# Kernel tuning notes

Hardware: AMD Instinct MI355X
Metric: run time of the kernel (lower is better)

Reference implementation:

```python
import jax, jax.numpy as jnp
import numpy as np

H = 128
B, N, K = 2, 16384, 16


def _gather_neighbors(a, idx):
    # a: (B,N,D), idx: (B,N,K) -> (B,N,K,D), per-batch gather along N
    return jax.vmap(lambda ab, ib: ab[ib])(a, idx)


def setup_inputs() -> dict:
    key = jax.random.key(0)
    ks = jax.random.split(key, 16)
    def lin(k, fan_in, shape):
        lim = 1.0 / np.sqrt(fan_in)
        return jax.random.uniform(k, shape, jnp.float32, -lim, lim)
    inp = {
        'h': jax.random.normal(ks[0], (B, N, H), jnp.float32),
        'x': jax.random.normal(ks[1], (B, N, 3), jnp.float32),
        'edge_idx': jax.random.randint(ks[2], (B, N, K), 0, N),
        # edge_mlp: Linear(2H+1->H), SiLU, Linear(H->H), SiLU
        'We1': lin(ks[3], 2 * H + 1, (2 * H + 1, H)), 'be1': lin(ks[4], 2 * H + 1, (H,)),
        'We2': lin(ks[5], H, (H, H)), 'be2': lin(ks[6], H, (H,)),
        # coord_mlp: Linear(H->H), SiLU, Linear(H->1, no bias)
        'Wc1': lin(ks[7], H, (H, H)), 'bc1': lin(ks[8], H, (H,)),
        'Wc2': lin(ks[9], H, (H, 1)),
        # node_mlp: Linear(2H->H), SiLU, Linear(H->H)
        'Wn1': lin(ks[10], 2 * H, (2 * H, H)), 'bn1': lin(ks[11], 2 * H, (H,)),
        'Wn2': lin(ks[12], H, (H, H)), 'bn2': lin(ks[13], H, (H,)),
    }
    return inp


def reference(h, x, edge_idx, We1, be1, We2, be2, Wc1, bc1, Wc2, Wn1, bn1, Wn2, bn2):
    k = edge_idx.shape[2]
    h_neigh = _gather_neighbors(h, edge_idx)          # (B,N,K,H)
    x_neigh = _gather_neighbors(x, edge_idx)          # (B,N,K,3)
    x_diff = x[:, :, None, :] - x_neigh               # (B,N,K,3)
    sq_dist = jnp.sum(x_diff * x_diff, axis=-1, keepdims=True)  # (B,N,K,1)
    h_i = jnp.broadcast_to(h[:, :, None, :], h_neigh.shape)
    edge_feat = jnp.concatenate([h_i, h_neigh, sq_dist], axis=-1)  # (B,N,K,2H+1)
    m_ij = jax.nn.silu(jax.nn.silu(edge_feat @ We1 + be1) @ We2 + be2)  # (B,N,K,H)
    coord_w = jax.nn.silu(m_ij @ Wc1 + bc1) @ Wc2     # (B,N,K,1)
    x_new = x + jnp.mean(x_diff * coord_w, axis=2)    # (B,N,3)
    m_i = jnp.sum(m_ij, axis=2)                       # (B,N,H)
    node_in = jnp.concatenate([h, m_i], axis=-1)      # (B,N,2H)
    h_new = jax.nn.silu(node_in @ Wn1 + bn1) @ Wn2 + bn2 + h
    return (h_new, x_new)
```

## Files before the change

kernel.cpp:

```cpp
#include <hip/hip_runtime.h>
#include <math.h>

#define H 128
#define KN 16
#define NN 16384
#define NB 8
#define EB 128

typedef short s16x8 __attribute__((ext_vector_type(8)));
typedef float f32x4 __attribute__((ext_vector_type(4)));

__device__ __forceinline__ float b2f(ushort u){
    union { uint i; float f; } v; v.i = ((uint)u) << 16; return v.f;
}
__device__ __forceinline__ ushort f2b(float f){
    union { float f; uint i; } v; v.f = f;
    uint r = v.i + 0x7fffu + ((v.i >> 16) & 1u);
    return (ushort)(r >> 16);
}
__device__ __forceinline__ float silu_f(float v){
    float e = __expf(-v);
    return v * __builtin_amdgcn_rcpf(1.0f + e);
}

__global__ __launch_bounds__(256) void pack_all(
    const float* __restrict__ We2, const float* __restrict__ Wc1,
    const float* __restrict__ Wn1, const float* __restrict__ Wn2,
    const float* __restrict__ We1,
    ushort* __restrict__ dWe2, ushort* __restrict__ dWc1,
    ushort* __restrict__ dWn1, ushort* __restrict__ dWn2,
    ushort* __restrict__ dW1p)
{
    int idx = blockIdx.x * 256 + threadIdx.x;
    int fid = idx >> 6, l = idx & 63;
    const float* src; ushort* dst; int Kt; int mode = 0; int lfid;
    if (fid < 32)       { src = We2; dst = dWe2; Kt = 4; lfid = fid; }
    else if (fid < 64)  { src = Wc1; dst = dWc1; Kt = 4; lfid = fid - 64 + 32 - 32; lfid = fid - 32; }
    else if (fid < 128) { src = Wn1; dst = dWn1; Kt = 8; lfid = fid - 64; }
    else if (fid < 160) { src = Wn2; dst = dWn2; Kt = 4; lfid = fid - 128; }
    else                { src = We1; dst = dW1p; Kt = 4; mode = 1; lfid = fid - 160; }
    int mt = lfid / Kt, kt = lfid % Kt;
    int m = mt * 16 + (l & 15);
    s16x8 ov;
#pragma unroll
    for (int e = 0; e < 8; e++){
        int k = kt * 32 + ((l >> 4) << 3) + e;
        float v;
        if (mode == 0) v = src[k * 128 + m];
        else           v = src[(k + ((m >= 128) ? 128 : 0)) * 128 + (m & 127)];
        ov[e] = (short)f2b(v);
    }
    *(s16x8*)(dst + (size_t)lfid * 512 + l * 8) = ov;
}

__global__ __launch_bounds__(256) void precompute_mfma(
    const float* __restrict__ h, const float* __restrict__ be1,
    const ushort* __restrict__ W1p,
    ushort* __restrict__ A, ushort* __restrict__ Bm)
{
    const int tid = threadIdx.x;
    const int w = tid >> 6, l = tid & 63, lg = l >> 4, li = l & 15;
    const int i0 = blockIdx.x * 64;

    f32x4 acc[4][4];
#pragma unroll
    for (int a = 0; a < 4; a++)
#pragma unroll
        for (int b = 0; b < 4; b++){ acc[a][b][0]=0.f; acc[a][b][1]=0.f; acc[a][b][2]=0.f; acc[a][b][3]=0.f; }

    for (int nt = 0; nt < 4; nt++){
        int node = i0 + nt * 16 + li;
        const float* hp = h + (size_t)node * 128 + lg * 8;
        s16x8 bfr[4];
#pragma unroll
        for (int kt = 0; kt < 4; kt++){
            float4 v0 = *(const float4*)(hp + kt * 32);
            float4 v1 = *(const float4*)(hp + kt * 32 + 4);
            s16x8 bf;
            bf[0]=(short)f2b(v0.x); bf[1]=(short)f2b(v0.y); bf[2]=(short)f2b(v0.z); bf[3]=(short)f2b(v0.w);
            bf[4]=(short)f2b(v1.x); bf[5]=(short)f2b(v1.y); bf[6]=(short)f2b(v1.z); bf[7]=(short)f2b(v1.w);
            bfr[kt] = bf;
        }
#pragma unroll
        for (int mtl = 0; mtl < 4; mtl++){
            int mt = w * 4 + mtl;
#pragma unroll
            for (int kt = 0; kt < 4; kt++){
                s16x8 af = *(const s16x8*)(W1p + (size_t)(mt * 4 + kt) * 512 + l * 8);
                acc[mtl][nt] = __builtin_amdgcn_mfma_f32_16x16x32_bf16(af, bfr[kt], acc[mtl][nt], 0, 0, 0);
            }
        }
    }
#pragma unroll
    for (int mtl = 0; mtl < 4; mtl++){
        int mt = w * 4 + mtl;
        int ccb = mt * 16 + lg * 4;
#pragma unroll
        for (int nt = 0; nt < 4; nt++){
            int node = i0 + nt * 16 + li;
            float b0=0.f,b1=0.f,b2=0.f,b3=0.f;
            if (ccb < 128){ float4 bb = *(const float4*)(be1 + ccb); b0=bb.x; b1=bb.y; b2=bb.z; b3=bb.w; }
            ushort o0 = f2b(acc[mtl][nt][0] + b0);
            ushort o1 = f2b(acc[mtl][nt][1] + b1);
            ushort o2 = f2b(acc[mtl][nt][2] + b2);
            ushort o3 = f2b(acc[mtl][nt][3] + b3);
            uint2 val = make_uint2((uint)o0 | ((uint)o1 << 16), (uint)o2 | ((uint)o3 << 16));
            ushort* dst = (ccb < 128) ? (A + (size_t)node * 128 + ccb)
                                      : (Bm + (size_t)node * 128 + (ccb - 128));
            *(uint2*)dst = val;
        }
    }
}

__global__ __launch_bounds__(256, 3) void egnn_fused(
    const float* __restrict__ h, const float* __restrict__ x,
    const int* __restrict__ edge_idx,
    const ushort* __restrict__ A, const ushort* __restrict__ Bm,
    const float* __restrict__ We1,
    const ushort* __restrict__ We2T, const float* __restrict__ be2,
    const ushort* __restrict__ Wc1T, const float* __restrict__ bc1,
    const float* __restrict__ Wc2,
    const ushort* __restrict__ Wn1T, const float* __restrict__ bn1,
    const ushort* __restrict__ Wn2T, const float* __restrict__ bn2,
    float* __restrict__ out, int BN)
{
    __shared__ ushort m_lds[EB * 128];
    __shared__ float  hsh[NB * 132];
    __shared__ ushort Ash[NB * 128];
    __shared__ float  msum[NB * 132];
    __shared__ ushort u_lds[16 * 128];
    __shared__ ushort w256sh[128];
    __shared__ float  sqd[EB];
    __shared__ float  xd[EB * 3];
    __shared__ float  cwvp[4][EB];
    __shared__ int    jgs[EB];

    const int tid = threadIdx.x;
    const int w = tid >> 6, l = tid & 63, lg = l >> 4, li = l & 15;
    const int i0 = blockIdx.x * NB;

    {
        int r = tid >> 5, c = (tid & 31) * 4;
        *(float4*)&hsh[r * 132 + c] = *(const float4*)&h[(size_t)(i0 + r) * 128 + c];
        if (tid < 128){
            int rr = tid >> 4, cc = (tid & 15) * 8;
            *(s16x8*)&Ash[rr * 128 + cc] = *(const s16x8*)&A[(size_t)(i0 + rr) * 128 + cc];
        } else {
            int t2 = tid - 128;
            w256sh[t2] = f2b(We1[256 * 128 + t2]);
            s16x8 z; for (int e = 0; e < 8; e++) z[e] = 0;
            *(s16x8*)&u_lds[(8 + (t2 >> 4)) * 128 + (t2 & 15) * 8] = z;
        }
        if (tid < EB){
            int e = tid;
            int i = i0 + (e >> 4);
            int b = i / NN;
            int jl = edge_idx[(size_t)i * KN + (e & 15)];
            int j = b * NN + jl;
            jgs[e] = j;
            float d0 = x[i*3+0] - x[j*3+0];
            float d1 = x[i*3+1] - x[j*3+1];
            float d2 = x[i*3+2] - x[j*3+2];
            xd[e*3+0] = d0; xd[e*3+1] = d1; xd[e*3+2] = d2;
            sqd[e] = d0*d0 + d1*d1 + d2*d2;
        }
    }
    __syncthreads();

    {
        const int e0 = w * 32;
#pragma unroll
        for (int nt = 0; nt < 2; nt++){
            int edge = e0 + nt * 16 + li;
            int nodel = edge >> 4;
            int j = jgs[edge];
            float sq = sqd[edge];
#pragma unroll
            for (int kt = 0; kt < 4; kt++){
                int c8 = kt * 32 + lg * 8;
                s16x8 bm = *(const s16x8*)&Bm[(size_t)j * 128 + c8];
                s16x8 av = *(const s16x8*)&Ash[nodel * 128 + c8];
                s16x8 wv = *(const s16x8*)&w256sh[c8];
                s16x8 ov;
#pragma unroll
                for (int e = 0; e < 8; e++){
                    float t = b2f((ushort)av[e]) + b2f((ushort)bm[e]) + sq * b2f((ushort)wv[e]);
                    ov[e] = (short)f2b(silu_f(t));
                }
                int blk = (kt * 4 + lg) ^ (edge & 7);
                *(s16x8*)&m_lds[edge * 128 + blk * 8] = ov;
            }
        }
    }
    __syncthreads();

    f32x4 acc[16];
#pragma unroll
    for (int q = 0; q < 16; q++){ acc[q][0]=0.f; acc[q][1]=0.f; acc[q][2]=0.f; acc[q][3]=0.f; }

#pragma unroll
    for (int kt = 0; kt < 4; kt++){
        s16x8 bfr[8];
#pragma unroll
        for (int nt = 0; nt < 8; nt++){
            int edge = nt * 16 + li;
            int blk = (kt * 4 + lg) ^ (edge & 7);
            bfr[nt] = *(const s16x8*)&m_lds[edge * 128 + blk * 8];
        }
#pragma unroll
        for (int mtl = 0; mtl < 2; mtl++){
            int mt = w * 2 + mtl;
            s16x8 af = *(const s16x8*)&We2T[(size_t)(mt * 4 + kt) * 512 + l * 8];
#pragma unroll
            for (int nt = 0; nt < 8; nt++)
                acc[mtl * 8 + nt] = __builtin_amdgcn_mfma_f32_16x16x32_bf16(af, bfr[nt], acc[mtl * 8 + nt], 0, 0, 0);
        }
    }
    __syncthreads();

#pragma unroll
    for (int mtl = 0; mtl < 2; mtl++){
        int mt = w * 2 + mtl;
        int cb = mt * 16 + lg * 4;
        float4 bb = *(const float4*)&be2[cb];
#pragma unroll
        for (int nt = 0; nt < 8; nt++){
            int edge = nt * 16 + li;
            f32x4 a = acc[mtl * 8 + nt];
            ushort o0 = f2b(silu_f(a[0] + bb.x));
            ushort o1 = f2b(silu_f(a[1] + bb.y));
            ushort o2 = f2b(silu_f(a[2] + bb.z));
            ushort o3 = f2b(silu_f(a[3] + bb.w));
            int blk = (mt * 2 + (lg >> 1)) ^ (edge & 7);
            uint2 val = make_uint2((uint)o0 | ((uint)o1 << 16), (uint)o2 | ((uint)o3 << 16));
            *(uint2*)&m_lds[edge * 128 + blk * 8 + (lg & 1) * 4] = val;
        }
    }
    {
        int nodel = l >> 3;
        int c0 = w * 32 + (l & 7) * 4;
        float s0=0.f, s1=0.f, s2=0.f, s3=0.f;
#pragma unroll
        for (int k = 0; k < 16; k++){
            int edge = nodel * 16 + k;
            int blk = (c0 >> 3) ^ (edge & 7);
            uint2 v = *(uint2*)&m_lds[edge * 128 + blk * 8 + (c0 & 4)];
            s0 += b2f((ushort)(v.x & 0xffff)); s1 += b2f((ushort)(v.x >> 16));
            s2 += b2f((ushort)(v.y & 0xffff)); s3 += b2f((ushort)(v.y >> 16));
        }
        float4 sv = make_float4(s0, s1, s2, s3);
        *(float4*)&msum[nodel * 132 + c0] = sv;
    }
    __syncthreads();

#pragma unroll
    for (int q = 0; q < 16; q++){ acc[q][0]=0.f; acc[q][1]=0.f; acc[q][2]=0.f; acc[q][3]=0.f; }
#pragma unroll
    for (int kt = 0; kt < 4; kt++){
        s16x8 bfr[8];
#pragma unroll
        for (int nt = 0; nt < 8; nt++){
            int edge = nt * 16 + li;
            int blk = (kt * 4 + lg) ^ (edge & 7);
            bfr[nt] = *(const s16x8*)&m_lds[edge * 128 + blk * 8];
        }
#pragma unroll
        for (int mtl = 0; mtl < 2; mtl++){
            int mt = w * 2 + mtl;
            s16x8 af = *(const s16x8*)&Wc1T[(size_t)(mt * 4 + kt) * 512 + l * 8];
#pragma unroll
            for (int nt = 0; nt < 8; nt++)
                acc[mtl * 8 + nt] = __builtin_amdgcn_mfma_f32_16x16x32_bf16(af, bfr[nt], acc[mtl * 8 + nt], 0, 0, 0);
        }
    }
    {
        float cwp[8];
#pragma unroll
        for (int nt = 0; nt < 8; nt++) cwp[nt] = 0.f;
#pragma unroll
        for (int mtl = 0; mtl < 2; mtl++){
            int mt = w * 2 + mtl;
            int cb = mt * 16 + lg * 4;
            float4 bc = *(const float4*)&bc1[cb];
            float4 wc = *(const float4*)&Wc2[cb];
#pragma unroll
            for (int nt = 0; nt < 8; nt++){
                f32x4 a = acc[mtl * 8 + nt];
                cwp[nt] += silu_f(a[0] + bc.x) * wc.x + silu_f(a[1] + bc.y) * wc.y
                         + silu_f(a[2] + bc.z) * wc.z + silu_f(a[3] + bc.w) * wc.w;
            }
        }
#pragma unroll
        for (int nt = 0; nt < 8; nt++){
            float v = cwp[nt];
            v += __shfl_xor(v, 16);
            v += __shfl_xor(v, 32);
            if (lg == 0) cwvp[w][nt * 16 + li] = v;
        }
    }

    {
        f32x4 acc3[2];
        acc3[0][0]=0.f; acc3[0][1]=0.f; acc3[0][2]=0.f; acc3[0][3]=0.f;
        acc3[1][0]=0.f; acc3[1][1]=0.f; acc3[1][2]=0.f; acc3[1][3]=0.f;
#pragma unroll
        for (int kt = 0; kt < 8; kt++){
            int node = li & 7;
            const float* bp = (kt < 4) ? (hsh + node * 132 + kt * 32 + lg * 8)
                                       : (msum + node * 132 + (kt - 4) * 32 + lg * 8);
            float4 v0 = *(const float4*)bp;
            float4 v1 = *(const float4*)(bp + 4);
            s16x8 bf;
            bf[0]=(short)f2b(v0.x); bf[1]=(short)f2b(v0.y); bf[2]=(short)f2b(v0.z); bf[3]=(short)f2b(v0.w);
            bf[4]=(short)f2b(v1.x); bf[5]=(short)f2b(v1.y); bf[6]=(short)f2b(v1.z); bf[7]=(short)f2b(v1.w);
#pragma unroll
            for (int mtl = 0; mtl < 2; mtl++){
                int mt = w * 2 + mtl;
                s16x8 af = *(const s16x8*)&Wn1T[(size_t)(mt * 8 + kt) * 512 + l * 8];
                acc3[mtl] = __builtin_amdgcn_mfma_f32_16x16x32_bf16(af, bf, acc3[mtl], 0, 0, 0);
            }
        }
#pragma unroll
        for (int mtl = 0; mtl < 2; mtl++){
            int mt = w * 2 + mtl;
            int cb = mt * 16 + lg * 4;
            float4 bb = *(const float4*)&bn1[cb];
            if (li < 8){
                f32x4 a = acc3[mtl];
                ushort o0 = f2b(silu_f(a[0] + bb.x));
                ushort o1 = f2b(silu_f(a[1] + bb.y));
                ushort o2 = f2b(silu_f(a[2] + bb.z));
                ushort o3 = f2b(silu_f(a[3] + bb.w));
                int blk = (mt * 2 + (lg >> 1)) ^ (li & 7);
                uint2 val = make_uint2((uint)o0 | ((uint)o1 << 16), (uint)o2 | ((uint)o3 << 16));
                *(uint2*)&u_lds[li * 128 + blk * 8 + (lg & 1) * 4] = val;
            }
        }
    }
    __syncthreads();

    if (tid < 24){
        int nd = tid / 3, d = tid % 3;
        float s = 0.f;
#pragma unroll
        for (int k = 0; k < 16; k++){
            int e = nd * 16 + k;
            s += xd[e * 3 + d] * (cwvp[0][e] + cwvp[1][e] + cwvp[2][e] + cwvp[3][e]);
        }
        int i = i0 + nd;
        out[(size_t)BN * H + (size_t)i * 3 + d] = x[(size_t)i * 3 + d] + s * (1.0f / 16.0f);
    }

    {
        f32x4 acc4[2];
        acc4[0][0]=0.f; acc4[0][1]=0.f; acc4[0][2]=0.f; acc4[0][3]=0.f;
        acc4[1][0]=0.f; acc4[1][1]=0.f; acc4[1][2]=0.f; acc4[1][3]=0.f;
#pragma unroll
        for (int kt = 0; kt < 4; kt++){
            int blk = (kt * 4 + lg) ^ (li & 7);
            s16x8 bf = *(const s16x8*)&u_lds[li * 128 + blk * 8];
#pragma unroll
            for (int mtl = 0; mtl < 2; mtl++){
                int mt = w * 2 + mtl;
                s16x8 af = *(const s16x8*)&Wn2T[(size_t)(mt * 4 + kt) * 512 + l * 8];
                acc4[mtl] = __builtin_amdgcn_mfma_f32_16x16x32_bf16(af, bf, acc4[mtl], 0, 0, 0);
            }
        }
#pragma unroll
        for (int mtl = 0; mtl < 2; mtl++){
            int mt = w * 2 + mtl;
            int cb = mt * 16 + lg * 4;
            if (li < 8){
                float4 bb = *(const float4*)&bn2[cb];
                float4 hv = *(const float4*)&hsh[li * 132 + cb];
                f32x4 a = acc4[mtl];
                float4 o;
                o.x = a[0] + bb.x + hv.x;
                o.y = a[1] + bb.y + hv.y;
                o.z = a[2] + bb.z + hv.z;
                o.w = a[3] + bb.w + hv.w;
                *(float4*)&out[(size_t)(i0 + li) * 128 + cb] = o;
            }
        }
    }
}

extern "C" void kernel_launch(void* const* d_in, const int* in_sizes, int n_in,
                              void* d_out, int out_size, void* d_ws, size_t ws_size,
                              hipStream_t stream) {
    const float* h        = (const float*)d_in[0];
    const float* x        = (const float*)d_in[1];
    const int*   edge_idx = (const int*)d_in[2];
    const float* We1      = (const float*)d_in[3];
    const float* be1      = (const float*)d_in[4];
    const float* We2      = (const float*)d_in[5];
    const float* be2      = (const float*)d_in[6];
    const float* Wc1      = (const float*)d_in[7];
    const float* bc1      = (const float*)d_in[8];
    const float* Wc2      = (const float*)d_in[9];
    const float* Wn1      = (const float*)d_in[10];
    const float* bn1      = (const float*)d_in[11];
    const float* Wn2      = (const float*)d_in[12];
    const float* bn2      = (const float*)d_in[13];
    float* out = (float*)d_out;

    const int BN = in_sizes[0] / H;

    ushort* A    = (ushort*)d_ws;
    ushort* Bm   = A + (size_t)BN * H;
    ushort* We2T = Bm + (size_t)BN * H;
    ushort* Wc1T = We2T + 32 * 512;
    ushort* Wn1T = Wc1T + 32 * 512;
    ushort* Wn2T = Wn1T + 64 * 512;
    ushort* W1pT = Wn2T + 32 * 512;

    pack_all<<<56, 256, 0, stream>>>(We2, Wc1, Wn1, Wn2, We1,
                                     We2T, Wc1T, Wn1T, Wn2T, W1pT);
    precompute_mfma<<<BN / 64, 256, 0, stream>>>(h, be1, W1pT, A, Bm);
    egnn_fused<<<BN / NB, 256, 0, stream>>>(h, x, edge_idx, A, Bm, We1,
                                            We2T, be2, Wc1T, bc1, Wc2,
                                            Wn1T, bn1, Wn2T, bn2, out, BN);
}
```

Before: 127.5 us.

## Shrink and alias LDS buffers, store bf16 staging, raise occupancy to 4 waves

```diff
diff --git a/kernel.cpp b/kernel.cpp
--- a/kernel.cpp
+++ b/kernel.cpp
@@ -1,4 +1,5 @@
 #include <hip/hip_runtime.h>
+#include <hip/hip_bf16.h>
 #include <math.h>
 
 #define H 128
@@ -6,17 +7,24 @@
 #define NN 16384
 #define NB 8
 #define EB 128
+#define HS 136
 
 typedef short s16x8 __attribute__((ext_vector_type(8)));
 typedef float f32x4 __attribute__((ext_vector_type(4)));
 
-__device__ __forceinline__ float b2f(ushort u){
-    union { uint i; float f; } v; v.i = ((uint)u) << 16; return v.f;
-}
-__device__ __forceinline__ ushort f2b(float f){
-    union { float f; uint i; } v; v.f = f;
-    uint r = v.i + 0x7fffu + ((v.i >> 16) & 1u);
-    return (ushort)(r >> 16);
+__device__ __forceinline__ float u2f_lo(uint u){
+    union { uint i; float f; } v; v.i = u << 16; return v.f;
+}
+__device__ __forceinline__ float u2f_hi(uint u){
+    union { uint i; float f; } v; v.i = u & 0xffff0000u; return v.f;
+}
+__device__ __forceinline__ uint pk2(float lo, float hi){
+    __hip_bfloat162 b = __float22bfloat162_rn(float2{lo, hi});
+    uint u; __builtin_memcpy(&u, &b, 4); return u;
+}
+__device__ __forceinline__ ushort f2b1(float f){
+    __hip_bfloat16 b = __float2bfloat16(f);
+    ushort u; __builtin_memcpy(&u, &b, 2); return u;
 }
 __device__ __forceinline__ float silu_f(float v){
     float e = __expf(-v);
@@ -35,7 +43,7 @@
     int fid = idx >> 6, l = idx & 63;
     const float* src; ushort* dst; int Kt; int mode = 0; int lfid;
     if (fid < 32)       { src = We2; dst = dWe2; Kt = 4; lfid = fid; }
-    else if (fid < 64)  { src = Wc1; dst = dWc1; Kt = 4; lfid = fid - 64 + 32 - 32; lfid = fid - 32; }
+    else if (fid < 64)  { src = Wc1; dst = dWc1; Kt = 4; lfid = fid - 32; }
     else if (fid < 128) { src = Wn1; dst = dWn1; Kt = 8; lfid = fid - 64; }
     else if (fid < 160) { src = Wn2; dst = dWn2; Kt = 4; lfid = fid - 128; }
     else                { src = We1; dst = dW1p; Kt = 4; mode = 1; lfid = fid - 160; }
@@ -48,7 +56,7 @@
         float v;
         if (mode == 0) v = src[k * 128 + m];
         else           v = src[(k + ((m >= 128) ? 128 : 0)) * 128 + (m & 127)];
-        ov[e] = (short)f2b(v);
+        ov[e] = (short)f2b1(v);
     }
     *(s16x8*)(dst + (size_t)lfid * 512 + l * 8) = ov;
 }
@@ -76,9 +84,9 @@
         for (int kt = 0; kt < 4; kt++){
             float4 v0 = *(const float4*)(hp + kt * 32);
             float4 v1 = *(const float4*)(hp + kt * 32 + 4);
-            s16x8 bf;
-            bf[0]=(short)f2b(v0.x); bf[1]=(short)f2b(v0.y); bf[2]=(short)f2b(v0.z); bf[3]=(short)f2b(v0.w);
-            bf[4]=(short)f2b(v1.x); bf[5]=(short)f2b(v1.y); bf[6]=(short)f2b(v1.z); bf[7]=(short)f2b(v1.w);
+            uint4 uu = make_uint4(pk2(v0.x, v0.y), pk2(v0.z, v0.w),
+                                  pk2(v1.x, v1.y), pk2(v1.z, v1.w));
+            s16x8 bf; __builtin_memcpy(&bf, &uu, 16);
             bfr[kt] = bf;
         }
 #pragma unroll
@@ -100,11 +108,8 @@
             int node = i0 + nt * 16 + li;
             float b0=0.f,b1=0.f,b2=0.f,b3=0.f;
             if (ccb < 128){ float4 bb = *(const float4*)(be1 + ccb); b0=bb.x; b1=bb.y; b2=bb.z; b3=bb.w; }
-            ushort o0 = f2b(acc[mtl][nt][0] + b0);
-            ushort o1 = f2b(acc[mtl][nt][1] + b1);
-            ushort o2 = f2b(acc[mtl][nt][2] + b2);
-            ushort o3 = f2b(acc[mtl][nt][3] + b3);
-            uint2 val = make_uint2((uint)o0 | ((uint)o1 << 16), (uint)o2 | ((uint)o3 << 16));
+            uint2 val = make_uint2(pk2(acc[mtl][nt][0] + b0, acc[mtl][nt][1] + b1),
+                                   pk2(acc[mtl][nt][2] + b2, acc[mtl][nt][3] + b3));
             ushort* dst = (ccb < 128) ? (A + (size_t)node * 128 + ccb)
                                       : (Bm + (size_t)node * 128 + (ccb - 128));
             *(uint2*)dst = val;
@@ -112,7 +117,7 @@
     }
 }
 
-__global__ __launch_bounds__(256, 3) void egnn_fused(
+__global__ __launch_bounds__(256, 4) void egnn_fused(
     const float* __restrict__ h, const float* __restrict__ x,
     const int* __restrict__ edge_idx,
     const ushort* __restrict__ A, const ushort* __restrict__ Bm,
@@ -124,16 +129,16 @@
     const ushort* __restrict__ Wn2T, const float* __restrict__ bn2,
     float* __restrict__ out, int BN)
 {
-    __shared__ ushort m_lds[EB * 128];
-    __shared__ float  hsh[NB * 132];
-    __shared__ ushort Ash[NB * 128];
-    __shared__ float  msum[NB * 132];
-    __shared__ ushort u_lds[16 * 128];
-    __shared__ ushort w256sh[128];
+    __shared__ __align__(16) ushort m_lds[EB * 128];
+    __shared__ __align__(16) uint   AshCw[512];
+    __shared__ __align__(16) ushort hsh_bf[NB * HS];
+    __shared__ __align__(16) ushort msum_bf[NB * HS];
+    __shared__ __align__(16) ushort w256sh[128];
     __shared__ float  sqd[EB];
-    __shared__ float  xd[EB * 3];
-    __shared__ float  cwvp[4][EB];
     __shared__ int    jgs[EB];
+
+    ushort* Ash = (ushort*)AshCw;
+    float (*cwvp)[EB] = (float(*)[EB])AshCw;
 
     const int tid = threadIdx.x;
     const int w = tid >> 6, l = tid & 63, lg = l >> 4, li = l & 15;
@@ -141,15 +146,14 @@
 
     {
         int r = tid >> 5, c = (tid & 31) * 4;
-        *(float4*)&hsh[r * 132 + c] = *(const float4*)&h[(size_t)(i0 + r) * 128 + c];
+        float4 hv = *(const float4*)&h[(size_t)(i0 + r) * 128 + c];
+        *(uint2*)&hsh_bf[r * HS + c] = make_uint2(pk2(hv.x, hv.y), pk2(hv.z, hv.w));
         if (tid < 128){
             int rr = tid >> 4, cc = (tid & 15) * 8;
-            *(s16x8*)&Ash[rr * 128 + cc] = *(const s16x8*)&A[(size_t)(i0 + rr) * 128 + cc];
+            *(uint4*)&Ash[rr * 128 + cc] = *(const uint4*)&A[(size_t)(i0 + rr) * 128 + cc];
         } else {
             int t2 = tid - 128;
-            w256sh[t2] = f2b(We1[256 * 128 + t2]);
-            s16x8 z; for (int e = 0; e < 8; e++) z[e] = 0;
-            *(s16x8*)&u_lds[(8 + (t2 >> 4)) * 128 + (t2 & 15) * 8] = z;
+            w256sh[t2] = f2b1(We1[256 * 128 + t2]);
         }
         if (tid < EB){
             int e = tid;
@@ -158,10 +162,9 @@
             int jl = edge_idx[(size_t)i * KN + (e & 15)];
             int j = b * NN + jl;
             jgs[e] = j;
-            float d0 = x[i*3+0] - x[j*3+0];
-            float d1 = x[i*3+1] - x[j*3+1];
-            float d2 = x[i*3+2] - x[j*3+2];
-            xd[e*3+0] = d0; xd[e*3+1] = d1; xd[e*3+2] = d2;
+            float d0 = x[(size_t)i*3+0] - x[(size_t)j*3+0];
+            float d1 = x[(size_t)i*3+1] - x[(size_t)j*3+1];
+            float d2 = x[(size_t)i*3+2] - x[(size_t)j*3+2];
             sqd[e] = d0*d0 + d1*d1 + d2*d2;
         }
     }
@@ -178,17 +181,21 @@
 #pragma unroll
             for (int kt = 0; kt < 4; kt++){
                 int c8 = kt * 32 + lg * 8;
-                s16x8 bm = *(const s16x8*)&Bm[(size_t)j * 128 + c8];
-                s16x8 av = *(const s16x8*)&Ash[nodel * 128 + c8];
-                s16x8 wv = *(const s16x8*)&w256sh[c8];
-                s16x8 ov;
-#pragma unroll
-                for (int e = 0; e < 8; e++){
-                    float t = b2f((ushort)av[e]) + b2f((ushort)bm[e]) + sq * b2f((ushort)wv[e]);
-                    ov[e] = (short)f2b(silu_f(t));
+                uint4 ub = *(const uint4*)&Bm[(size_t)j * 128 + c8];
+                uint4 ua = *(const uint4*)&Ash[nodel * 128 + c8];
+                uint4 uw = *(const uint4*)&w256sh[c8];
+                uint ov[4];
+                const uint* pa = (const uint*)&ua;
+                const uint* pb = (const uint*)&ub;
+                const uint* pw = (const uint*)&uw;
+#pragma unroll
+                for (int p = 0; p < 4; p++){
+                    float tlo = fmaf(sq, u2f_lo(pw[p]), u2f_lo(pa[p]) + u2f_lo(pb[p]));
+                    float thi = fmaf(sq, u2f_hi(pw[p]), u2f_hi(pa[p]) + u2f_hi(pb[p]));
+                    ov[p] = pk2(silu_f(tlo), silu_f(thi));
                 }
                 int blk = (kt * 4 + lg) ^ (edge & 7);
-                *(s16x8*)&m_lds[edge * 128 + blk * 8] = ov;
+                *(uint4*)&m_lds[edge * 128 + blk * 8] = make_uint4(ov[0], ov[1], ov[2], ov[3]);
             }
         }
     }
@@ -198,6 +205,7 @@
 #pragma unroll
     for (int q = 0; q < 16; q++){ acc[q][0]=0.f; acc[q][1]=0.f; acc[q][2]=0.f; acc[q][3]=0.f; }
 
+    __builtin_amdgcn_s_setprio(1);
 #pragma unroll
     for (int kt = 0; kt < 4; kt++){
         s16x8 bfr[8];
@@ -216,6 +224,7 @@
                 acc[mtl * 8 + nt] = __builtin_amdgcn_mfma_f32_16x16x32_bf16(af, bfr[nt], acc[mtl * 8 + nt], 0, 0, 0);
         }
     }
+    __builtin_amdgcn_s_setprio(0);
     __syncthreads();
 
 #pragma unroll
@@ -227,15 +236,13 @@
         for (int nt = 0; nt < 8; nt++){
             int edge = nt * 16 + li;
             f32x4 a = acc[mtl * 8 + nt];
-            ushort o0 = f2b(silu_f(a[0] + bb.x));
-            ushort o1 = f2b(silu_f(a[1] + bb.y));
-            ushort o2 = f2b(silu_f(a[2] + bb.z));
-            ushort o3 = f2b(silu_f(a[3] + bb.w));
+            uint2 val = make_uint2(pk2(silu_f(a[0] + bb.x), silu_f(a[1] + bb.y)),
+                                   pk2(silu_f(a[2] + bb.z), silu_f(a[3] + bb.w)));
             int blk = (mt * 2 + (lg >> 1)) ^ (edge & 7);
-            uint2 val = make_uint2((uint)o0 | ((uint)o1 << 16), (uint)o2 | ((uint)o3 << 16));
             *(uint2*)&m_lds[edge * 128 + blk * 8 + (lg & 1) * 4] = val;
         }
     }
+    __syncthreads();
     {
         int nodel = l >> 3;
         int c0 = w * 32 + (l & 7) * 4;
@@ -245,16 +252,16 @@
             int edge = nodel * 16 + k;
             int blk = (c0 >> 3) ^ (edge & 7);
             uint2 v = *(uint2*)&m_lds[edge * 128 + blk * 8 + (c0 & 4)];
-            s0 += b2f((ushort)(v.x & 0xffff)); s1 += b2f((ushort)(v.x >> 16));
-            s2 += b2f((ushort)(v.y & 0xffff)); s3 += b2f((ushort)(v.y >> 16));
-        }
-        float4 sv = make_float4(s0, s1, s2, s3);
-        *(float4*)&msum[nodel * 132 + c0] = sv;
+            s0 += u2f_lo(v.x); s1 += u2f_hi(v.x);
+            s2 += u2f_lo(v.y); s3 += u2f_hi(v.y);
+        }
+        *(uint2*)&msum_bf[nodel * HS + c0] = make_uint2(pk2(s0, s1), pk2(s2, s3));
     }
     __syncthreads();
 
 #pragma unroll
     for (int q = 0; q < 16; q++){ acc[q][0]=0.f; acc[q][1]=0.f; acc[q][2]=0.f; acc[q][3]=0.f; }
+    __builtin_amdgcn_s_setprio(1);
 #pragma unroll
     for (int kt = 0; kt < 4; kt++){
         s16x8 bfr[8];
@@ -273,6 +280,9 @@
                 acc[mtl * 8 + nt] = __builtin_amdgcn_mfma_f32_16x16x32_bf16(af, bfr[nt], acc[mtl * 8 + nt], 0, 0, 0);
         }
     }
+    __builtin_amdgcn_s_setprio(0);
+    __syncthreads();
+
     {
         float cwp[8];
 #pragma unroll
@@ -303,16 +313,12 @@
         f32x4 acc3[2];
         acc3[0][0]=0.f; acc3[0][1]=0.f; acc3[0][2]=0.f; acc3[0][3]=0.f;
         acc3[1][0]=0.f; acc3[1][1]=0.f; acc3[1][2]=0.f; acc3[1][3]=0.f;
+        int node = li & 7;
 #pragma unroll
         for (int kt = 0; kt < 8; kt++){
-            int node = li & 7;
-            const float* bp = (kt < 4) ? (hsh + node * 132 + kt * 32 + lg * 8)
-                                       : (msum + node * 132 + (kt - 4) * 32 + lg * 8);
-            float4 v0 = *(const float4*)bp;
-            float4 v1 = *(const float4*)(bp + 4);
-            s16x8 bf;
-            bf[0]=(short)f2b(v0.x); bf[1]=(short)f2b(v0.y); bf[2]=(short)f2b(v0.z); bf[3]=(short)f2b(v0.w);
-            bf[4]=(short)f2b(v1.x); bf[5]=(short)f2b(v1.y); bf[6]=(short)f2b(v1.z); bf[7]=(short)f2b(v1.w);
+            const ushort* bp = (kt < 4) ? &hsh_bf[node * HS + kt * 32 + lg * 8]
+                                        : &msum_bf[node * HS + (kt - 4) * 32 + lg * 8];
+            s16x8 bf = *(const s16x8*)bp;
 #pragma unroll
             for (int mtl = 0; mtl < 2; mtl++){
                 int mt = w * 2 + mtl;
@@ -325,30 +331,30 @@
             int mt = w * 2 + mtl;
             int cb = mt * 16 + lg * 4;
             float4 bb = *(const float4*)&bn1[cb];
+            uint o01 = 0, o23 = 0;
             if (li < 8){
                 f32x4 a = acc3[mtl];
-                ushort o0 = f2b(silu_f(a[0] + bb.x));
-                ushort o1 = f2b(silu_f(a[1] + bb.y));
-                ushort o2 = f2b(silu_f(a[2] + bb.z));
-                ushort o3 = f2b(silu_f(a[3] + bb.w));
-                int blk = (mt * 2 + (lg >> 1)) ^ (li & 7);
-                uint2 val = make_uint2((uint)o0 | ((uint)o1 << 16), (uint)o2 | ((uint)o3 << 16));
-                *(uint2*)&u_lds[li * 128 + blk * 8 + (lg & 1) * 4] = val;
-            }
+                o01 = pk2(silu_f(a[0] + bb.x), silu_f(a[1] + bb.y));
+                o23 = pk2(silu_f(a[2] + bb.z), silu_f(a[3] + bb.w));
+            }
+            int blk = (mt * 2 + (lg >> 1)) ^ (li & 7);
+            *(uint2*)&m_lds[li * 128 + blk * 8 + (lg & 1) * 4] = make_uint2(o01, o23);
         }
     }
     __syncthreads();
 
     if (tid < 24){
         int nd = tid / 3, d = tid % 3;
+        int i = i0 + nd;
+        float xi = x[(size_t)i * 3 + d];
         float s = 0.f;
 #pragma unroll
         for (int k = 0; k < 16; k++){
             int e = nd * 16 + k;
-            s += xd[e * 3 + d] * (cwvp[0][e] + cwvp[1][e] + cwvp[2][e] + cwvp[3][e]);
-        }
-        int i = i0 + nd;
-        out[(size_t)BN * H + (size_t)i * 3 + d] = x[(size_t)i * 3 + d] + s * (1.0f / 16.0f);
+            float cw = cwvp[0][e] + cwvp[1][e] + cwvp[2][e] + cwvp[3][e];
+            s += (xi - x[(size_t)jgs[e] * 3 + d]) * cw;
+        }
+        out[(size_t)BN * H + (size_t)i * 3 + d] = xi + s * (1.0f / 16.0f);
     }
 
     {
@@ -358,7 +364,7 @@
 #pragma unroll
         for (int kt = 0; kt < 4; kt++){
             int blk = (kt * 4 + lg) ^ (li & 7);
-            s16x8 bf = *(const s16x8*)&u_lds[li * 128 + blk * 8];
+            s16x8 bf = *(const s16x8*)&m_lds[li * 128 + blk * 8];
 #pragma unroll
             for (int mtl = 0; mtl < 2; mtl++){
                 int mt = w * 2 + mtl;
@@ -372,7 +378,7 @@
             int cb = mt * 16 + lg * 4;
             if (li < 8){
                 float4 bb = *(const float4*)&bn2[cb];
-                float4 hv = *(const float4*)&hsh[li * 132 + cb];
+                float4 hv = *(const float4*)&h[(size_t)(i0 + li) * 128 + cb];
                 f32x4 a = acc4[mtl];
                 float4 o;
                 o.x = a[0] + bb.x + hv.x;
```

New measurement: 140.4 us. +10.1%, slower.
